# Kernel optimization log

Hardware: AMD Instinct MI355X
Metric: run time of the kernel (lower is better)

## Reference

```python
import jax, jax.numpy as jnp
import numpy as np

B, S, D_IN, D_OUT = 4, 4096, 256, 256

def setup_inputs() -> dict:
    key = jax.random.key(0)
    ks = jax.random.split(key, 7)
    scale = 1.0 / np.sqrt(D_IN)
    return {
        "x": jax.random.normal(ks[0], (B, S, D_IN), dtype=jnp.float32),
        "Wq": jax.random.uniform(ks[1], (D_IN, D_OUT), jnp.float32, -scale, scale),
        "bq": jax.random.uniform(ks[2], (D_OUT,), jnp.float32, -scale, scale),
        "Wk": jax.random.uniform(ks[3], (D_IN, D_OUT), jnp.float32, -scale, scale),
        "bk": jax.random.uniform(ks[4], (D_OUT,), jnp.float32, -scale, scale),
        "Wv": jax.random.uniform(ks[5], (D_IN, D_OUT), jnp.float32, -scale, scale),
        "bv": jax.random.uniform(ks[6], (D_OUT,), jnp.float32, -scale, scale),
    }

def reference(x, Wq, bq, Wk, bk, Wv, bv):
    # QKV projections: [B, S, D_OUT]
    q = jnp.einsum("bsd,de->bse", x, Wq) + bq
    k = jnp.einsum("bsd,de->bse", x, Wk) + bk
    v = jnp.einsum("bsd,de->bse", x, Wv) + bv
    # Scaled dot-product attention; full [B, S, S] scores as in the original.
    scores = jnp.einsum("bqe,bke->bqk", q, k) / jnp.sqrt(jnp.asarray(q.shape[-1], q.dtype))
    attn = jax.nn.softmax(scores, axis=-1)
    return jnp.einsum("bqk,bke->bqe", attn, v)
```

## Files before the change

kernel.cpp:

```cpp
#include <hip/hip_runtime.h>
#include <stdint.h>

typedef unsigned short u16;
typedef long long i64;
typedef __attribute__((ext_vector_type(4))) float f32x4;
typedef __attribute__((ext_vector_type(8))) short bf16x8;
typedef __attribute__((ext_vector_type(4))) int i32x4;
typedef __attribute__((ext_vector_type(2))) unsigned int u32x2;

#define SEQ 4096
#define DIM 256
#define QS4 0.36067376f

__device__ __forceinline__ u16 f2bf(float f) {
  union { float f; uint32_t u; } v; v.f = f;
  uint32_t r = (v.u + 0x7FFFu + ((v.u >> 16) & 1u)) >> 16;
  return (u16)r;
}

__device__ __forceinline__ float bf2f(u16 u) {
  union { uint32_t u; float f; } v; v.u = ((uint32_t)u) << 16;
  return v.f;
}

__device__ __forceinline__ uint8_t f2fp8(float f) {
  return (uint8_t)__builtin_amdgcn_cvt_pk_fp8_f32(f, 0.f, 0, false);
}

__device__ __forceinline__ void gload_lds16(const void* g, void* lds) {
  __builtin_amdgcn_global_load_lds(
      (const __attribute__((address_space(1))) uint32_t*)g,
      (__attribute__((address_space(3))) uint32_t*)lds, 16, 0, 0);
}

__device__ __forceinline__ f32x4 mfma8(i64 a, i64 b, f32x4 c) {
  return __builtin_amdgcn_mfma_f32_16x16x32_fp8_fp8(a, b, c, 0, 0, 0);
}

__global__ __launch_bounds__(256) void wt_kernel(const float* __restrict__ Wq,
                                                 const float* __restrict__ Wk,
                                                 const float* __restrict__ Wv,
                                                 u16* __restrict__ wt) {
  int b = blockIdx.x;
  int w = b >> 8;
  int n = b & 255;
  const float* W = (w == 0) ? Wq : ((w == 1) ? Wk : Wv);
  float scale = (w == 0) ? QS4 : ((w == 1) ? 0.25f : 1.0f);
  int k = threadIdx.x;
  wt[(w * 256 + n) * 256 + k] = f2bf(W[k * 256 + n] * scale);
}

__global__ __launch_bounds__(256) void qkv_kernel(
    const float* __restrict__ x, const float* __restrict__ bq,
    const float* __restrict__ bk, const float* __restrict__ bv,
    const u16* __restrict__ wt, uint8_t* __restrict__ qs,
    uint8_t* __restrict__ kk, char* __restrict__ vt) {
  __shared__ __align__(16) char lds_b[65536];
  __shared__ __align__(16) u16 lds_v[4096];
  __shared__ float lds_bias[768];
  int tid = threadIdx.x;
  int w = tid >> 6, l = tid & 63;
  int a = l & 15, g = l >> 4;
  int rowbase = blockIdx.x * 64;

  lds_bias[tid] = bq[tid] * QS4;
  lds_bias[256 + tid] = bk[tid] * 0.25f;
  lds_bias[512 + tid] = bv[tid];

  uint32_t wso[8];
#pragma unroll
  for (int j = 0; j < 8; ++j) {
    uint32_t inst = w * 8 + j;
    uint32_t flat = inst * 1024 + l * 16;
    uint32_t row = flat >> 9;
    uint32_t c5 = (flat >> 4) & 31;
    uint32_t sc = (c5 & ~7u) | ((c5 ^ row) & 7u);
    wso[j] = row * 512 + sc * 16;
  }
  uint32_t bro[8];
#pragma unroll
  for (int ks = 0; ks < 8; ++ks) {
    uint32_t c5 = ks * 4 + g;
    uint32_t sc = (c5 & ~7u) | ((c5 ^ (a & 7u)) & 7u);
    bro[ks] = (uint32_t)a * 512 + sc * 16;
  }

#pragma unroll
  for (int j = 0; j < 8; ++j)
    gload_lds16((const char*)wt + wso[j], lds_b + (w * 8 + j) * 1024);

  bf16x8 afr[8];
  {
    int row = rowbase + w * 16 + a;
    const f32x4* xr4 = (const f32x4*)(x + (size_t)row * 256);
#pragma unroll
    for (int ks = 0; ks < 8; ++ks) {
      int q4 = ks * 8 + g * 2;
      f32x4 lo = xr4[q4], hi = xr4[q4 + 1];
      union { bf16x8 s; u16 u[8]; } fr;
      fr.u[0] = f2bf(lo[0]); fr.u[1] = f2bf(lo[1]);
      fr.u[2] = f2bf(lo[2]); fr.u[3] = f2bf(lo[3]);
      fr.u[4] = f2bf(hi[0]); fr.u[5] = f2bf(hi[1]);
      fr.u[6] = f2bf(hi[2]); fr.u[7] = f2bf(hi[3]);
      afr[ks] = fr.s;
    }
  }

  int cur = 0;
  for (int it = 0; it < 12; ++it) {
    asm volatile("s_waitcnt vmcnt(0) lgkmcnt(0)" ::: "memory");
    __builtin_amdgcn_s_barrier();
    __builtin_amdgcn_sched_barrier(0);
    if (it < 11) {
#pragma unroll
      for (int j = 0; j < 8; ++j)
        gload_lds16((const char*)wt + (size_t)(it + 1) * 32768 + wso[j],
                    lds_b + (cur ^ 1) * 32768 + (w * 8 + j) * 1024);
    }
    int w3 = it >> 2, qn = it & 3;
    f32x4 acc[4];
#pragma unroll
    for (int n0 = 0; n0 < 4; ++n0) acc[n0] = (f32x4){0.f, 0.f, 0.f, 0.f};
#pragma unroll
    for (int ks = 0; ks < 8; ++ks) {
#pragma unroll
      for (int n0 = 0; n0 < 4; ++n0) {
        bf16x8 bfr = *(const bf16x8*)(lds_b + cur * 32768 + bro[ks] + n0 * 8192);
        acc[n0] = __builtin_amdgcn_mfma_f32_16x16x32_bf16(afr[ks], bfr, acc[n0], 0, 0, 0);
      }
    }
    if (w3 < 2) {
      uint8_t* out8 = (w3 == 0) ? qs : kk;
#pragma unroll
      for (int n0 = 0; n0 < 4; ++n0) {
        int col = qn * 64 + n0 * 16 + a;
        float bb = lds_bias[w3 * 256 + col];
#pragma unroll
        for (int r = 0; r < 4; ++r) {
          int row = rowbase + w * 16 + g * 4 + r;
          out8[(size_t)row * 256 + col] = f2fp8(acc[n0][r] + bb);
        }
      }
    } else {
#pragma unroll
      for (int n0 = 0; n0 < 4; ++n0) {
        int col = qn * 64 + n0 * 16 + a;
        float bb = lds_bias[512 + col];
        int dl = n0 * 16 + a;
#pragma unroll
        for (int r = 0; r < 4; ++r) {
          int m = w * 16 + g * 4 + r;
          uint32_t byteoff =
              (uint32_t)dl * 128 + ((((uint32_t)m >> 3) ^ ((uint32_t)dl & 7)) << 4) + (m & 7) * 2;
          *(u16*)((char*)lds_v + byteoff) = f2bf(acc[n0][r] + bb);
        }
      }
      asm volatile("s_waitcnt lgkmcnt(0)" ::: "memory");
      __builtin_amdgcn_s_barrier();
      {
        int dl = tid >> 2;
        size_t base = (size_t)blockIdx.x * 32768 + (size_t)(qn * 64 + dl) * 128;
#pragma unroll
        for (int cc = 0; cc < 2; ++cc) {
          uint32_t c = (tid & 3) + cc * 4;
          i32x4 vd = *(const i32x4*)((const char*)lds_v + dl * 128 + ((c ^ (dl & 7)) << 4));
          *(i32x4*)(vt + base + c * 16) = vd;
        }
      }
    }
    cur ^= 1;
  }
}

#define VVB 32768u
#define PVB 98304u

#define PV_STEP(SLOT)                                                          \
  {                                                                            \
    bf16x8 pfr[2][2];                                                          \
    _Pragma("unroll") for (int mt = 0; mt < 2; ++mt)                           \
    _Pragma("unroll") for (int j2 = 0; j2 < 2; ++j2)                           \
        pfr[mt][j2] = *(const bf16x8*)(lds + PVB + (SLOT) * 16384 + pro[j2] +  \
                                       mt * 2048);                             \
    __builtin_amdgcn_s_setprio(1);                                             \
    if (sub == 0) {                                                            \
      _Pragma("unroll") for (int mt = 0; mt < 2; ++mt)                         \
      _Pragma("unroll") for (int j2 = 0; j2 < 2; ++j2)                         \
          lacc[mt] = __builtin_amdgcn_mfma_f32_16x16x32_bf16(pfr[mt][j2], ones,\
                                                             lacc[mt], 0, 0, 0); \
    }                                                                          \
    _Pragma("unroll") for (int d0 = 0; d0 < 4; ++d0)                           \
    _Pragma("unroll") for (int j2 = 0; j2 < 2; ++j2) {                         \
      bf16x8 vfr = *(const bf16x8*)(lds + VVB + (SLOT) * 32768 + vro[j2] +     \
                                    d0 * 2048);                                \
      o[0][d0] = __builtin_amdgcn_mfma_f32_16x16x32_bf16(pfr[0][j2], vfr, o[0][d0], 0, 0, 0); \
      o[1][d0] = __builtin_amdgcn_mfma_f32_16x16x32_bf16(pfr[1][j2], vfr, o[1][d0], 0, 0, 0); \
    }                                                                          \
    __builtin_amdgcn_s_setprio(0);                                             \
  }

#define TILE(CUR, DO_PV, DO_K)                                                 \
  {                                                                            \
    asm volatile("s_waitcnt vmcnt(0) lgkmcnt(0)" ::: "memory");                \
    __builtin_amdgcn_s_barrier();                                              \
    __builtin_amdgcn_sched_barrier(0);                                         \
    gload_lds16(vstp + vso[0], lds + VVB + (CUR) * 32768 + (w * 2 + 0) * 1024); \
    gload_lds16(vstp + vso[1], lds + VVB + (CUR) * 32768 + (w * 2 + 1) * 1024); \
    if (DO_K)                                                                  \
      gload_lds16(kstp + kso0, lds + ((CUR) ^ 1) * 16384 + w * 1024);          \
    kstp += 16384;                                                             \
    vstp += 32768;                                                             \
    f32x4 sc[2];                                                               \
    sc[0] = (f32x4){0.f, 0.f, 0.f, 0.f};                                       \
    sc[1] = (f32x4){0.f, 0.f, 0.f, 0.f};                                       \
    __builtin_amdgcn_s_setprio(1);                                             \
    _Pragma("unroll") for (int j = 0; j < 8; ++j) {                            \
      i64 kfr = *(const i64*)(lds + (CUR) * 16384 + kro[j]);                   \
      sc[0] = mfma8(kfr, qfr[0][j], sc[0]);                                    \
      sc[1] = mfma8(kfr, qfr[1][j], sc[1]);                                    \
    }                                                                          \
    __builtin_amdgcn_s_setprio(0);                                             \
    _Pragma("unroll") for (int mt = 0; mt < 2; ++mt) {                         \
      float e0 = exp2f(sc[mt][0]);                                             \
      float e1 = exp2f(sc[mt][1]);                                             \
      float e2 = exp2f(sc[mt][2]);                                             \
      float e3 = exp2f(sc[mt][3]);                                             \
      uint32_t p0 = (uint32_t)f2bf(e0) | ((uint32_t)f2bf(e1) << 16);           \
      uint32_t p1 = (uint32_t)f2bf(e2) | ((uint32_t)f2bf(e3) << 16);           \
      u32x2 pk = {p0, p1};                                                     \
      *(u32x2*)(lds + PVB + (CUR) * 16384 + pwo + mt * 2048) = pk;             \
    }                                                                          \
    if (DO_PV) PV_STEP((CUR) ^ 1)                                              \
  }

__global__ __launch_bounds__(1024, 1) void attn_kernel(
    const uint8_t* __restrict__ qs, const uint8_t* __restrict__ kk,
    const char* __restrict__ vt, float* __restrict__ out,
    u16* __restrict__ pOB, float* __restrict__ pl, int split) {
  __shared__ __align__(16) char lds[131072];
  int tid = threadIdx.x;
  int w = tid >> 6, l = tid & 63;
  int a = l & 15, g = l >> 4;
  int qq = w >> 2, sub = w & 3;
  int bx = blockIdx.x;
  int h, batch, qt;
  if (split == 2) { h = bx & 1; batch = (bx >> 1) & 3; qt = bx >> 3; }
  else            { h = 0;      batch = (bx >> 1) & 3; qt = ((bx >> 3) << 1) | (bx & 1); }
  int ntHalf = (split == 2) ? 16 : 32;

  uint32_t a7 = a & 7;
  uint32_t kro[8], vro[2], pro[2], pwo, kso0, vso[2];
  {
    uint32_t row = (uint32_t)(sub * 16 + a);
#pragma unroll
    for (int j = 0; j < 8; ++j) {
      uint32_t c4 = j * 2 + (g >> 1);
      kro[j] = row * 256 + (((c4 & ~7u) | ((c4 ^ a7) & 7u)) << 4) + (g & 1) * 8;
    }
  }
#pragma unroll
  for (int j2 = 0; j2 < 2; ++j2)
    vro[j2] = (uint32_t)(sub * 64 + a) * 128 +
              ((((uint32_t)(j2 * 4 + g)) ^ a7) << 4);
  {
    uint32_t q = (uint32_t)(qq * 32 + a);
#pragma unroll
    for (int j2 = 0; j2 < 2; ++j2)
      pro[j2] = q * 128 + ((((uint32_t)(j2 * 4 + g)) ^ a7) << 4);
    uint32_t tg = (uint32_t)(sub * 2 + (g >> 1));
    pwo = q * 128 + ((tg ^ a7) << 4) + (g & 1) * 8;
  }
  {
    uint32_t flat = (uint32_t)w * 1024 + l * 16;
    uint32_t row = flat >> 8, c4 = (flat >> 4) & 15;
    kso0 = row * 256 + (((c4 & ~7u) | ((c4 ^ (row & 7u)) & 7u)) << 4);
  }
#pragma unroll
  for (int j = 0; j < 2; ++j) {
    uint32_t inst = w * 2 + j, flat = inst * 1024 + l * 16;
    uint32_t row = flat >> 7, c3 = (flat >> 4) & 7;
    vso[j] = row * 128 + ((c3 ^ (row & 7)) << 4);
  }

  i64 qfr[2][8];
  {
    const uint8_t* qp = qs + (size_t)(batch * SEQ + qt * 128) * 256;
#pragma unroll
    for (int mt = 0; mt < 2; ++mt)
#pragma unroll
      for (int j = 0; j < 8; ++j)
        qfr[mt][j] = *(const i64*)(qp + (size_t)(qq * 32 + mt * 16 + a) * 256 +
                                   j * 32 + g * 8);
  }

  f32x4 o[2][4];
  f32x4 lacc[2];
#pragma unroll
  for (int mt = 0; mt < 2; ++mt) {
    lacc[mt] = (f32x4){0.f, 0.f, 0.f, 0.f};
#pragma unroll
    for (int d0 = 0; d0 < 4; ++d0) o[mt][d0] = (f32x4){0.f, 0.f, 0.f, 0.f};
  }
  const short ob = (short)0x3F80;
  bf16x8 ones = {ob, ob, ob, ob, ob, ob, ob, ob};

  const uint8_t* kstp = kk + (size_t)batch * SEQ * 256 + (size_t)h * 2048 * 256;
  const char* vstp = vt + (size_t)batch * 64 * 32768 + (size_t)h * 32 * 32768;

  gload_lds16(kstp + kso0, lds + w * 1024);
  kstp += 16384;

  TILE(0, false, true)
  for (int tp = 0; tp < ntHalf - 1; ++tp) {
    TILE(1, true, true)
    TILE(0, true, true)
  }
  TILE(1, true, false)

  asm volatile("s_waitcnt vmcnt(0) lgkmcnt(0)" ::: "memory");
  __builtin_amdgcn_s_barrier();
  __builtin_amdgcn_sched_barrier(0);
  PV_STEP(1)

  size_t obase = (size_t)(batch * SEQ + qt * 128 + qq * 32) * 256 + sub * 64;
  if (h == 0) {
#pragma unroll
    for (int mt = 0; mt < 2; ++mt)
#pragma unroll
      for (int r = 0; r < 4; ++r) {
#pragma unroll
        for (int d0 = 0; d0 < 4; ++d0)
          out[obase + (size_t)(mt * 16 + g * 4 + r) * 256 + d0 * 16 + a] = o[mt][d0][r];
      }
  } else {
#pragma unroll
    for (int mt = 0; mt < 2; ++mt)
#pragma unroll
      for (int r = 0; r < 4; ++r) {
#pragma unroll
        for (int d0 = 0; d0 < 4; ++d0)
          pOB[obase + (size_t)(mt * 16 + g * 4 + r) * 256 + d0 * 16 + a] =
              f2bf(o[mt][d0][r]);
      }
  }
  if (a == 0 && sub == 0) {
#pragma unroll
    for (int mt = 0; mt < 2; ++mt)
#pragma unroll
      for (int r = 0; r < 4; ++r)
        pl[h * 16384 + (batch * 32 + qt) * 128 + qq * 32 + mt * 16 + g * 4 + r] =
            lacc[mt][r];
  }
}

__global__ __launch_bounds__(256) void combine_kernel(float* __restrict__ out,
                                                      const u16* __restrict__ pOB,
                                                      const float* __restrict__ pl,
                                                      int split) {
  int b = blockIdx.x;
  int tid = threadIdx.x;
  int batch = b >> 12;
  int rem = b & 4095;
  int qt = rem >> 7, ql = rem & 127;
  size_t idx = (size_t)b * 256 + tid;
  int li = (batch * 32 + qt) * 128 + ql;
  float lA = pl[li];
  float v;
  if (split == 2) {
    float lB = pl[16384 + li];
    v = (out[idx] + bf2f(pOB[idx])) / (lA + lB);
  } else {
    v = out[idx] / lA;
  }
  out[idx] = v;
}

extern "C" void kernel_launch(void* const* d_in, const int* in_sizes, int n_in,
                              void* d_out, int out_size, void* d_ws, size_t ws_size,
                              hipStream_t stream) {
  const float* x = (const float*)d_in[0];
  const float* Wq = (const float*)d_in[1];
  const float* bq = (const float*)d_in[2];
  const float* Wk = (const float*)d_in[3];
  const float* bk = (const float*)d_in[4];
  const float* Wv = (const float*)d_in[5];
  const float* bv = (const float*)d_in[6];
  char* ws = (char*)d_ws;
  u16* wt = (u16*)ws;
  uint8_t* qs = (uint8_t*)(ws + 0x60000);
  uint8_t* kk = (uint8_t*)(ws + 0x460000);
  char* vt = ws + 0x860000;
  float* pl = (float*)(ws + 0x1060000);
  u16* pOB = (u16*)(ws + 0x1080000);
  int split = (ws_size >= 0x1880000ull) ? 2 : 1;
  wt_kernel<<<dim3(768), dim3(256), 0, stream>>>(Wq, Wk, Wv, wt);
  qkv_kernel<<<dim3(256), dim3(256), 0, stream>>>(x, bq, bk, bv, wt, qs, kk, vt);
  attn_kernel<<<dim3(split * 128), dim3(1024), 0, stream>>>(qs, kk, vt, (float*)d_out,
                                                            pOB, pl, split);
  combine_kernel<<<dim3(16384), dim3(256), 0, stream>>>((float*)d_out, pOB, pl, split);
}
```

Baseline: 110.0 us.

## Fuse split-KV combine into attention kernel via last-arriver atomic flag

Drops the separate combine kernel. Each of the two split-KV halves writes its bf16 partial output and row sums to its own slab, then bumps a per-tile atomic counter, and whichever block arrives second merges both partials, normalises, and writes the final output. The non-split path now normalises in place using row sums shared through LDS. This removes one kernel launch and a full read/write pass over the output, but adds a memset, a wider workspace requirement, and a serialised merge tail in the second-arriving block.

```diff
diff --git a/kernel.cpp b/kernel.cpp
--- a/kernel.cpp
+++ b/kernel.cpp
@@ -236,7 +236,8 @@
 __global__ __launch_bounds__(1024, 1) void attn_kernel(
     const uint8_t* __restrict__ qs, const uint8_t* __restrict__ kk,
     const char* __restrict__ vt, float* __restrict__ out,
-    u16* __restrict__ pOB, float* __restrict__ pl, int split) {
+    u16* __restrict__ pOB, float* __restrict__ pl,
+    uint32_t* __restrict__ flags, int split) {
   __shared__ __align__(16) char lds[131072];
   int tid = threadIdx.x;
   int w = tid >> 6, l = tid & 63;
@@ -323,56 +324,75 @@
   PV_STEP(1)
 
   size_t obase = (size_t)(batch * SEQ + qt * 128 + qq * 32) * 256 + sub * 64;
-  if (h == 0) {
+  float* lsh = (float*)lds;
+  if (split == 2) {
+    u16* slab = pOB + (size_t)h * 0x400000;
 #pragma unroll
     for (int mt = 0; mt < 2; ++mt)
 #pragma unroll
+      for (int r = 0; r < 4; ++r)
+#pragma unroll
+        for (int d0 = 0; d0 < 4; ++d0)
+          slab[obase + (size_t)(mt * 16 + g * 4 + r) * 256 + d0 * 16 + a] =
+              f2bf(o[mt][d0][r]);
+    if (sub == 0 && a == 0) {
+#pragma unroll
+      for (int mt = 0; mt < 2; ++mt)
+#pragma unroll
+        for (int r = 0; r < 4; ++r) {
+          int row = qq * 32 + mt * 16 + g * 4 + r;
+          lsh[row] = lacc[mt][r];
+          pl[h * 16384 + (batch * 32 + qt) * 128 + row] = lacc[mt][r];
+        }
+    }
+    asm volatile("s_waitcnt vmcnt(0) lgkmcnt(0)" ::: "memory");
+    __builtin_amdgcn_s_barrier();
+    if (tid == 0) {
+      __threadfence();
+      uint32_t old = atomicAdd(&flags[batch * 32 + qt], 1u);
+      *(volatile int*)(lds + 512) = (int)old;
+    }
+    __syncthreads();
+    int old = *(volatile int*)(lds + 512);
+    if (old == 1) {
+      __threadfence();
+      const u16* oslab = pOB + (size_t)(h ^ 1) * 0x400000;
+      const float* opl = pl + (h ^ 1) * 16384;
+#pragma unroll
+      for (int mt = 0; mt < 2; ++mt)
+#pragma unroll
+        for (int r = 0; r < 4; ++r) {
+          int row = qq * 32 + mt * 16 + g * 4 + r;
+          float inv = 1.0f / (lsh[row] + opl[(batch * 32 + qt) * 128 + row]);
+#pragma unroll
+          for (int d0 = 0; d0 < 4; ++d0) {
+            size_t idx = obase + (size_t)(mt * 16 + g * 4 + r) * 256 + d0 * 16 + a;
+            out[idx] = (bf2f(f2bf(o[mt][d0][r])) + bf2f(oslab[idx])) * inv;
+          }
+        }
+    }
+  } else {
+    if (sub == 0 && a == 0) {
+#pragma unroll
+      for (int mt = 0; mt < 2; ++mt)
+#pragma unroll
+        for (int r = 0; r < 4; ++r)
+          lsh[qq * 32 + mt * 16 + g * 4 + r] = lacc[mt][r];
+    }
+    asm volatile("s_waitcnt lgkmcnt(0)" ::: "memory");
+    __builtin_amdgcn_s_barrier();
+#pragma unroll
+    for (int mt = 0; mt < 2; ++mt)
+#pragma unroll
       for (int r = 0; r < 4; ++r) {
+        int row = qq * 32 + mt * 16 + g * 4 + r;
+        float inv = 1.0f / lsh[row];
 #pragma unroll
         for (int d0 = 0; d0 < 4; ++d0)
-          out[obase + (size_t)(mt * 16 + g * 4 + r) * 256 + d0 * 16 + a] = o[mt][d0][r];
+          out[obase + (size_t)(mt * 16 + g * 4 + r) * 256 + d0 * 16 + a] =
+              o[mt][d0][r] * inv;
       }
-  } else {
-#pragma unroll
-    for (int mt = 0; mt < 2; ++mt)
-#pragma unroll
-      for (int r = 0; r < 4; ++r) {
-#pragma unroll
-        for (int d0 = 0; d0 < 4; ++d0)
-          pOB[obase + (size_t)(mt * 16 + g * 4 + r) * 256 + d0 * 16 + a] =
-              f2bf(o[mt][d0][r]);
-      }
-  }
-  if (a == 0 && sub == 0) {
-#pragma unroll
-    for (int mt = 0; mt < 2; ++mt)
-#pragma unroll
-      for (int r = 0; r < 4; ++r)
-        pl[h * 16384 + (batch * 32 + qt) * 128 + qq * 32 + mt * 16 + g * 4 + r] =
-            lacc[mt][r];
-  }
-}
-
-__global__ __launch_bounds__(256) void combine_kernel(float* __restrict__ out,
-                                                      const u16* __restrict__ pOB,
-                                                      const float* __restrict__ pl,
-                                                      int split) {
-  int b = blockIdx.x;
-  int tid = threadIdx.x;
-  int batch = b >> 12;
-  int rem = b & 4095;
-  int qt = rem >> 7, ql = rem & 127;
-  size_t idx = (size_t)b * 256 + tid;
-  int li = (batch * 32 + qt) * 128 + ql;
-  float lA = pl[li];
-  float v;
-  if (split == 2) {
-    float lB = pl[16384 + li];
-    v = (out[idx] + bf2f(pOB[idx])) / (lA + lB);
-  } else {
-    v = out[idx] / lA;
-  }
-  out[idx] = v;
+  }
 }
 
 extern "C" void kernel_launch(void* const* d_in, const int* in_sizes, int n_in,
@@ -391,11 +411,12 @@
   uint8_t* kk = (uint8_t*)(ws + 0x460000);
   char* vt = ws + 0x860000;
   float* pl = (float*)(ws + 0x1060000);
-  u16* pOB = (u16*)(ws + 0x1080000);
-  int split = (ws_size >= 0x1880000ull) ? 2 : 1;
+  uint32_t* flags = (uint32_t*)(ws + 0x1080000);
+  u16* pOB = (u16*)(ws + 0x1090000);
+  int split = (ws_size >= 0x2090000ull) ? 2 : 1;
   wt_kernel<<<dim3(768), dim3(256), 0, stream>>>(Wq, Wk, Wv, wt);
   qkv_kernel<<<dim3(256), dim3(256), 0, stream>>>(x, bq, bk, bv, wt, qs, kk, vt);
+  if (split == 2) hipMemsetAsync(flags, 0, 512, stream);
   attn_kernel<<<dim3(split * 128), dim3(1024), 0, stream>>>(qs, kk, vt, (float*)d_out,
-                                                            pOB, pl, split);
-  combine_kernel<<<dim3(16384), dim3(256), 0, stream>>>((float*)d_out, pOB, pl, split);
-}
+                                                            pOB, pl, flags, split);
+}
```

Result: slower. 183.9 us (+67.2%).
